# Optimization experiments

Hardware: AMD Instinct MI355X
Metric: run time of the kernel (lower is better)

## Reference

```python
import math
import jax, jax.numpy as jnp
import numpy as np
from jax.scipy.special import xlogy, gammaln

DIM = 768
HEADS = 8
DIM_KEY = 64
DIM_VALUE = 64
NUM_REL_POS_FEATURES = 192
B = 2
N = 2048


def get_positional_embed(seq_len, feature_size):
    # distances: [-n+1, ..., n-1], length 2n-1
    dist = jnp.arange(-seq_len + 1, seq_len).astype(jnp.float32)
    ad = jnp.abs(dist)[:, None]  # [2n-1, 1]
    nb = feature_size // 6  # num basis per class (3 fns, doubled by sign concat)

    # exponential
    max_range = math.log(seq_len) / math.log(2.0)
    half_life = 2.0 ** jnp.linspace(3.0, max_range, nb)  # min_half_life = 3.0
    f_exp = jnp.exp(-math.log(2.0) / half_life[None, :] * ad)

    # central mask
    widths = 2.0 ** jnp.arange(1, nb + 1).astype(jnp.float32) - 1.0
    f_cm = (widths[None, :] > ad).astype(jnp.float32)

    # gamma pdf
    stddev = seq_len / (2.0 * nb)
    start_mean = seq_len / nb
    mean = jnp.linspace(start_mean, float(seq_len), nb)[None, :]
    conc = (mean / stddev) ** 2
    rate = mean / (stddev ** 2)
    log_unnorm = xlogy(conc - 1.0, ad) - rate * ad
    log_norm = gammaln(conc) - conc * jnp.log(rate)
    prob = jnp.exp(log_unnorm - log_norm) + 1e-8
    f_g = prob / jnp.max(prob, axis=-1, keepdims=True)

    emb = jnp.concatenate([f_exp, f_cm, f_g], axis=-1)  # [2n-1, 3*nb]
    emb = jnp.concatenate([emb, jnp.sign(dist)[:, None] * emb], axis=-1)  # [2n-1, 6*nb]
    return emb


def relative_shift(x):
    # x: [b, h, t1, 2*t1 - 1] -> [b, h, t1, t1] via pad/reshape trick
    b, h, t1, t2 = x.shape
    x = jnp.pad(x, ((0, 0), (0, 0), (0, 0), (1, 0)))  # [b,h,t1,t2+1]
    x = x.reshape(b, h, t2 + 1, t1)[:, :, 1:, :].reshape(b, h, t1, t2)
    return x[..., : (t2 + 2) // 2]


def setup_inputs() -> dict:
    key = jax.random.key(0)
    ks = jax.random.split(key, 9)
    dk, dv, h = DIM_KEY, DIM_VALUE, HEADS
    s_in = 1.0 / math.sqrt(DIM)
    s_rel = 1.0 / math.sqrt(NUM_REL_POS_FEATURES)
    s_out = 1.0 / math.sqrt(dv * h)
    return {
        "x": jax.random.normal(ks[0], (B, N, DIM), dtype=jnp.float32),
        # weights stored [in, out] (torch Linear weight transposed)
        "Wq": jax.random.normal(ks[1], (DIM, dk * h), dtype=jnp.float32) * s_in,
        "Wk": jax.random.normal(ks[2], (DIM, dk * h), dtype=jnp.float32) * s_in,
        "Wv": jax.random.normal(ks[3], (DIM, dv * h), dtype=jnp.float32) * s_in,
        "Wrel": jax.random.normal(ks[4], (NUM_REL_POS_FEATURES, dk * h), dtype=jnp.float32) * s_rel,
        # module inits to_out at zeros; use random values for a meaningful baseline
        "Wout": jax.random.normal(ks[5], (dv * h, DIM), dtype=jnp.float32) * s_out,
        "b_out": jax.random.normal(ks[6], (DIM,), dtype=jnp.float32) * 0.01,
        "rel_content_bias": jax.random.normal(ks[7], (1, h, 1, dk), dtype=jnp.float32),
        "rel_pos_bias": jax.random.normal(ks[8], (1, h, 1, dk), dtype=jnp.float32),
    }


def reference(x, Wq, Wk, Wv, Wrel, Wout, b_out, rel_content_bias, rel_pos_bias):
    b, n, _ = x.shape
    h, dk = HEADS, DIM_KEY
    scale = dk ** -0.5

    q = (x @ Wq).reshape(b, n, h, dk).transpose(0, 2, 1, 3) * scale  # [b,h,n,dk]
    k = (x @ Wk).reshape(b, n, h, dk).transpose(0, 2, 1, 3)
    v = (x @ Wv).reshape(b, n, h, -1).transpose(0, 2, 1, 3)  # [b,h,n,dv]

    content_logits = jnp.einsum('bhid,bhjd->bhij', q + rel_content_bias, k)

    positions = get_positional_embed(n, NUM_REL_POS_FEATURES)  # [2n-1, F]
    rel_k = (positions @ Wrel).reshape(2 * n - 1, h, dk).transpose(1, 0, 2)  # [h,2n-1,dk]
    rel_logits = jnp.einsum('bhid,hjd->bhij', q + rel_pos_bias, rel_k)  # [b,h,n,2n-1]
    rel_logits = relative_shift(rel_logits)  # [b,h,n,n]

    attn = jax.nn.softmax(content_logits + rel_logits, axis=-1)
    out = jnp.einsum('bhij,bhjd->bhid', attn, v)  # [b,h,n,dv]
    out = out.transpose(0, 2, 1, 3).reshape(b, n, -1)  # [b,n,h*dv]
    return out @ Wout + b_out
```

## Files before the change

kernel.cpp:

```cpp
#include <hip/hip_runtime.h>
#include <hip/hip_bf16.h>
#include <math.h>
#include <stdint.h>

typedef __hip_bfloat16 bf16;
typedef __attribute__((ext_vector_type(8))) short short8;
typedef __attribute__((ext_vector_type(4))) float f32x4;

#define SEQ   2048
#define NPOS  4095
#define DIMM  768
#define HEADS 8
#define DK    64
#define HD    512
#define BATCH 2
#define BH    16
#define ROWS  4096

#define OB_RELK  ((size_t)0)
#define OB_QC    ((size_t)4194304)
#define OB_QP    ((size_t)8388608)
#define OB_K     ((size_t)12582912)
#define OB_V     ((size_t)16777216)
#define OB_OH    ((size_t)20971520)
#define OB_EMBH  OB_OH
#define OB_EMBL  ((size_t)(OB_OH + 1572864))
#define OB_XH    ((size_t)25165824)
#define OB_XL    ((size_t)31457280)
#define OB_WQKVH ((size_t)37748736)
#define OB_WQKVL ((size_t)40108032)
#define OB_OP    ((size_t)25165824)
#define OB_LP    ((size_t)41943040)
#define OB_WOH   ((size_t)42467328)
#define OB_WOL   ((size_t)43253760)
#define OB_WRH   ((size_t)44040192)
#define OB_WRL   ((size_t)44236800)

__device__ __forceinline__ unsigned f2bf(float f) {
  unsigned u = __float_as_uint(f);
  return (u + 0x7fffu + ((u >> 16) & 1u)) >> 16;
}
__device__ __forceinline__ void split2(float v, unsigned& hb, unsigned& lb) {
  hb = f2bf(v);
  const float back = __uint_as_float(hb << 16);
  lb = f2bf(v - back);
}

__device__ __forceinline__ void cp16(const short* g, short* l) {
  __builtin_amdgcn_global_load_lds(
      (__attribute__((address_space(1))) void*)(uintptr_t)(g),
      (__attribute__((address_space(3))) void*)(uint32_t)(uintptr_t)(l),
      16, 0, 0);
}

__global__ __launch_bounds__(256) void prep_all(
    const float* __restrict__ x,
    const float* __restrict__ Wq, const float* __restrict__ Wk,
    const float* __restrict__ Wv, const float* __restrict__ Wout,
    const float* __restrict__ Wrel,
    short* __restrict__ eh, short* __restrict__ el,
    short* __restrict__ xh, short* __restrict__ xl,
    short* __restrict__ wqkvh, short* __restrict__ wqkvl,
    short* __restrict__ woh, short* __restrict__ wol,
    short* __restrict__ wrh, short* __restrict__ wrl) {
  __shared__ float tile[32][33];
  const int blk = blockIdx.x;
  const int t = threadIdx.x;

  if (blk < 512) {
    const int row = blk * 8 + (t >> 5);
    const int j   = t & 31;
    if (row >= NPOS) {
      for (int c = j; c < 192; c += 32) { eh[(size_t)row * 192 + c] = 0; el[(size_t)row * 192 + c] = 0; }
      return;
    }
    const float dist = (float)(row - (SEQ - 1));
    const float ad   = fabsf(dist);
    const float hl    = exp2f(3.0f + 8.0f * (float)j / 31.0f);
    const float f_exp = exp2f(-ad / hl);
    const float width = exp2f((float)(j + 1)) - 1.0f;
    const float f_cm  = (width > ad) ? 1.0f : 0.0f;
    float prob;
    if (ad > 0.0f) {
      const float c   = 4.0f * (float)((j + 1) * (j + 1));
      const float r   = (float)(j + 1) / 16.0f;
      const float lu  = (c - 1.0f) * logf(ad) - r * ad;
      const float ln_ = lgammaf(c) - c * logf(r);
      prob = expf(lu - ln_) + 1e-8f;
    } else {
      prob = 1e-8f;
    }
    float mx = prob;
    for (int off = 16; off; off >>= 1) mx = fmaxf(mx, __shfl_xor(mx, off, 32));
    const float f_g = prob / mx;
    const float s = (dist > 0.f) ? 1.f : ((dist < 0.f) ? -1.f : 0.f);
    const float vals[6] = {f_exp, f_cm, f_g, s * f_exp, s * f_cm, s * f_g};
    short* ph = eh + (size_t)row * 192;
    short* pl = el + (size_t)row * 192;
#pragma unroll
    for (int q = 0; q < 6; q++) {
      unsigned hb, lb;
      split2(vals[q], hb, lb);
      ph[q * 32 + j] = (short)hb;
      pl[q * 32 + j] = (short)lb;
    }
    return;
  }

  if (blk < 3584) {
    const int i = (blk - 512) * 256 + t;
    const float4 v = ((const float4*)x)[i];
    unsigned h0, l0, h1, l1, h2, l2, h3, l3;
    split2(v.x, h0, l0); split2(v.y, h1, l1); split2(v.z, h2, l2); split2(v.w, h3, l3);
    *(uint2*)&xh[(size_t)i * 4] = make_uint2(h0 | (h1 << 16), h2 | (h3 << 16));
    *(uint2*)&xl[(size_t)i * 4] = make_uint2(l0 | (l1 << 16), l2 | (l3 << 16));
    return;
  }

  const float* src; short* dh; short* dl; int R, C, local;
  if (blk < 3968)      { local = blk - 3584; src = Wq;   dh = wqkvh;               dl = wqkvl;               R = DIMM; C = HD; }
  else if (blk < 4352) { local = blk - 3968; src = Wk;   dh = wqkvh + 512 * DIMM;  dl = wqkvl + 512 * DIMM;  R = DIMM; C = HD; }
  else if (blk < 4736) { local = blk - 4352; src = Wv;   dh = wqkvh + 1024 * DIMM; dl = wqkvl + 1024 * DIMM; R = DIMM; C = HD; }
  else if (blk < 5120) { local = blk - 4736; src = Wout; dh = woh;  dl = wol;  R = HD;  C = DIMM; }
  else                 { local = blk - 5120; src = Wrel; dh = wrh;  dl = wrl;  R = 192; C = HD; }
  const int ctiles = C / 32;
  const int c0 = (local % ctiles) * 32, r0 = (local / ctiles) * 32;
  {
    const int lr = t >> 3, lc = (t & 7) * 4;
    const float4 v = *(const float4*)&src[(size_t)(r0 + lr) * C + c0 + lc];
    tile[lr][lc] = v.x; tile[lr][lc + 1] = v.y; tile[lr][lc + 2] = v.z; tile[lr][lc + 3] = v.w;
  }
  __syncthreads();
  const int nn = t >> 3, kb = (t & 7) * 4;
  unsigned hb[4], lb[4];
#pragma unroll
  for (int e = 0; e < 4; e++) split2(tile[kb + e][nn], hb[e], lb[e]);
  const size_t o = (size_t)(c0 + nn) * R + r0 + kb;
  *(uint2*)&dh[o] = make_uint2(hb[0] | (hb[1] << 16), hb[2] | (hb[3] << 16));
  *(uint2*)&dl[o] = make_uint2(lb[0] | (lb[1] << 16), lb[2] | (lb[3] << 16));
}

__global__ __launch_bounds__(256) void gemm_qr(
    const short* __restrict__ xh, const short* __restrict__ xl,
    const short* __restrict__ wqkvh, const short* __restrict__ wqkvl,
    const short* __restrict__ eh, const short* __restrict__ el,
    const short* __restrict__ wrh, const short* __restrict__ wrl,
    const float* __restrict__ cb, const float* __restrict__ pb,
    bf16* __restrict__ oq, bf16* __restrict__ oqp,
    bf16* __restrict__ ok, short* __restrict__ vtw,
    bf16* __restrict__ relk) {
  __shared__ short AsH[2][128][32];
  __shared__ short AsL[2][128][32];
  __shared__ short BsH[2][128][32];
  __shared__ short BsL[2][128][32];

  const int bx = blockIdx.x;
  const bool isq = bx < 384;
  const int lbx = isq ? bx : bx - 384;
  const int mt = lbx & 31, ntile = lbx >> 5;
  const int m0 = mt * 128, n0 = ntile * 128;
  const int KD = isq ? DIMM : 192;
  const short* Ah = isq ? xh : eh;
  const short* Al = isq ? xl : el;
  const short* Bh = isq ? wqkvh : wrh;
  const short* Bl = isq ? wqkvl : wrl;

  const int t = threadIdx.x, lane = t & 63, w = t >> 6;
  const int quad = lane >> 4, l15 = lane & 15;
  const int wm = (w >> 1) * 64, wn = (w & 1) * 64;

  const int srow = w * 32 + (lane >> 2);
  const int skof = (lane & 3) * 8;

  auto STAGE = [&](int bb, int k0) {
#pragma unroll
    for (int c = 0; c < 2; c++) {
      const size_t ra = (size_t)(m0 + srow + c * 16) * KD + k0 + skof;
      const size_t rb = (size_t)(n0 + srow + c * 16) * KD + k0 + skof;
      cp16(&Ah[ra], &AsH[bb][w * 32 + c * 16][0]);
      cp16(&Al[ra], &AsL[bb][w * 32 + c * 16][0]);
      cp16(&Bh[rb], &BsH[bb][w * 32 + c * 16][0]);
      cp16(&Bl[rb], &BsL[bb][w * 32 + c * 16][0]);
    }
  };

  f32x4 acc[4][4];
#pragma unroll
  for (int i = 0; i < 4; i++)
#pragma unroll
    for (int j = 0; j < 4; j++) acc[i][j] = (f32x4){0.f, 0.f, 0.f, 0.f};

  STAGE(0, 0);
  __syncthreads();

  int bb = 0;
  for (int k0 = 0; k0 < KD; k0 += 32) {
    if (k0 + 32 < KD) STAGE(bb ^ 1, k0 + 32);

    short8 amh[4], aml[4], bnh[4], bnl[4];
#pragma unroll
    for (int i = 0; i < 4; i++) {
      amh[i] = *(const short8*)&AsH[bb][wm + i * 16 + l15][quad * 8];
      aml[i] = *(const short8*)&AsL[bb][wm + i * 16 + l15][quad * 8];
      bnh[i] = *(const short8*)&BsH[bb][wn + i * 16 + l15][quad * 8];
      bnl[i] = *(const short8*)&BsL[bb][wn + i * 16 + l15][quad * 8];
    }
#pragma unroll
    for (int i = 0; i < 4; i++) {
#pragma unroll
      for (int j = 0; j < 4; j++) {
        acc[i][j] = __builtin_amdgcn_mfma_f32_16x16x32_bf16(amh[i], bnh[j], acc[i][j], 0, 0, 0);
        acc[i][j] = __builtin_amdgcn_mfma_f32_16x16x32_bf16(amh[i], bnl[j], acc[i][j], 0, 0, 0);
        acc[i][j] = __builtin_amdgcn_mfma_f32_16x16x32_bf16(aml[i], bnh[j], acc[i][j], 0, 0, 0);
      }
    }

    __syncthreads();
    bb ^= 1;
  }

  if (isq) {
    const int sel = ntile >> 2;
    if (sel == 2) {
#pragma unroll
      for (int i = 0; i < 4; i++) {
#pragma unroll
        for (int j = 0; j < 4; j++) {
          const int n = n0 + wn + j * 16 + l15;
          const int hd_ = n & 511, hh = hd_ >> 6, d = hd_ & 63;
          const int m = m0 + wm + i * 16 + quad * 4;
          const int b = m >> 11, s = m & 2047;
          const int s_swz = s ^ ((d & 7) << 3);
          const uint2 pk = make_uint2(
              f2bf(acc[i][j][0]) | (f2bf(acc[i][j][1]) << 16),
              f2bf(acc[i][j][2]) | (f2bf(acc[i][j][3]) << 16));
          *(uint2*)&vtw[(((size_t)(b * HEADS + hh) * DK + d) * SEQ) + s_swz] = pk;
        }
      }
    } else {
#pragma unroll
      for (int i = 0; i < 4; i++) {
#pragma unroll
        for (int j = 0; j < 4; j++) {
          const int n = n0 + wn + j * 16 + l15;
          const int hd_ = n & 511, hh = hd_ >> 6, d = hd_ & 63;
#pragma unroll
          for (int g = 0; g < 4; g++) {
            const int m = m0 + wm + i * 16 + quad * 4 + g;
            const int b = m >> 11, s = m & 2047;
            const size_t idx = (((size_t)(b * HEADS + hh) * SEQ) + s) * DK + d;
            const float v = acc[i][j][g];
            if (sel == 0) {
              const float sv = v * 0.125f;
              oq[idx]  = __float2bfloat16(sv + cb[hh * DK + d]);
              oqp[idx] = __float2bfloat16(sv + pb[hh * DK + d]);
            } else {
              ok[idx] = __float2bfloat16(v);
            }
          }
        }
      }
    }
  } else {
#pragma unroll
    for (int i = 0; i < 4; i++) {
#pragma unroll
      for (int j = 0; j < 4; j++) {
        const int n = n0 + wn + j * 16 + l15;
        const int hh = n >> 6, d = n & 63;
#pragma unroll
        for (int g = 0; g < 4; g++) {
          const int m = m0 + wm + i * 16 + quad * 4 + g;
          if (m < NPOS)
            relk[((size_t)hh * NPOS + m) * DK + (d ^ ((m & 7) << 3))] =
                __float2bfloat16(acc[i][j][g]);
        }
      }
    }
  }
}

__global__ __launch_bounds__(256) void out_gemm(
    const short* __restrict__ Ahp,
    const short* __restrict__ Bhp, const short* __restrict__ Blp,
    const float* __restrict__ bias, float* __restrict__ ofp) {
  __shared__ short AsH[2][128][32];
  __shared__ short BsH[2][128][32];
  __shared__ short BsL[2][128][32];

  const int t = threadIdx.x, lane = t & 63, w = t >> 6;
  const int quad = lane >> 4, l15 = lane & 15;
  const int wm = (w >> 1) * 64, wn = (w & 1) * 64;
  const int m0 = blockIdx.x * 128, n0 = blockIdx.y * 128;
  const int srow = w * 32 + (lane >> 2);
  const int skof = (lane & 3) * 8;

  auto STAGE = [&](int bb, int k0) {
#pragma unroll
    for (int c = 0; c < 2; c++) {
      const size_t ra = (size_t)(m0 + srow + c * 16) * HD + k0 + skof;
      const size_t rb = (size_t)(n0 + srow + c * 16) * HD + k0 + skof;
      cp16(&Ahp[ra], &AsH[bb][w * 32 + c * 16][0]);
      cp16(&Bhp[rb], &BsH[bb][w * 32 + c * 16][0]);
      cp16(&Blp[rb], &BsL[bb][w * 32 + c * 16][0]);
    }
  };

  f32x4 acc[4][4];
#pragma unroll
  for (int i = 0; i < 4; i++)
#pragma unroll
    for (int j = 0; j < 4; j++) acc[i][j] = (f32x4){0.f, 0.f, 0.f, 0.f};

  STAGE(0, 0);
  __syncthreads();

  int bb = 0;
  for (int k0 = 0; k0 < HD; k0 += 32) {
    if (k0 + 32 < HD) STAGE(bb ^ 1, k0 + 32);

    short8 amh[4], bnh[4], bnl[4];
#pragma unroll
    for (int i = 0; i < 4; i++) {
      amh[i] = *(const short8*)&AsH[bb][wm + i * 16 + l15][quad * 8];
      bnh[i] = *(const short8*)&BsH[bb][wn + i * 16 + l15][quad * 8];
      bnl[i] = *(const short8*)&BsL[bb][wn + i * 16 + l15][quad * 8];
    }
#pragma unroll
    for (int i = 0; i < 4; i++) {
#pragma unroll
      for (int j = 0; j < 4; j++) {
        acc[i][j] = __builtin_amdgcn_mfma_f32_16x16x32_bf16(amh[i], bnh[j], acc[i][j], 0, 0, 0);
        acc[i][j] = __builtin_amdgcn_mfma_f32_16x16x32_bf16(amh[i], bnl[j], acc[i][j], 0, 0, 0);
      }
    }

    __syncthreads();
    bb ^= 1;
  }

#pragma unroll
  for (int i = 0; i < 4; i++) {
#pragma unroll
    for (int j = 0; j < 4; j++) {
      const int n = n0 + wn + j * 16 + l15;
      const float bv = bias[n];
#pragma unroll
      for (int g = 0; g < 4; g++) {
        const int m = m0 + wm + i * 16 + quad * 4 + g;
        ofp[(size_t)m * DIMM + n] = acc[i][j][g] + bv;
      }
    }
  }
}

__global__ __launch_bounds__(256) void attn_mfma4(
    const short* __restrict__ qc, const short* __restrict__ qp,
    const short* __restrict__ kg, const short* __restrict__ vt,
    const short* __restrict__ relk,
    float* __restrict__ Op, float* __restrict__ Lp) {
  __shared__ __align__(16) short RelR[128 * 64];
  __shared__ __align__(16) short VtB[2][64 * 64];
  __shared__ __align__(16) short Pw[4][16][64];

  const int bid = blockIdx.x;
  const int swz = (bid & 7) * 128 + (bid >> 3);
  const int i0  = (swz & 31) * 64;
  const int bh  = (swz >> 5) & 15;
  const int z   = swz >> 9;
  const int h   = bh & 7;
  const int jb  = z * (SEQ / 2);

  const int t    = threadIdx.x;
  const int lane = t & 63;
  const int w    = t >> 6;
  const int quad = lane >> 4;
  const int l15  = lane & 15;
  const int x    = (l15 & 7) << 3;

  short8 qcA[2], qpA[2];
  {
    const size_t qrow = ((size_t)bh * SEQ + i0 + w * 16 + l15) * DK + quad * 8;
    qcA[0] = *(const short8*)(qc + qrow);
    qcA[1] = *(const short8*)(qc + qrow + 32);
    qpA[0] = *(const short8*)(qp + qrow);
    qpA[1] = *(const short8*)(qp + qrow + 32);
  }

  int idxg[4]; bool selg[4];
#pragma unroll
  for (int g = 0; g < 4; g++) {
    const int r = quad * 4 + g;
    idxg[g] = (((lane & 48) | ((l15 + 15 - r) & 15)) << 2);
    selg[g] = (l15 <= r);
  }

  short8 ones8;
#pragma unroll
  for (int e = 0; e < 8; e++) ones8[e] = (short)0x3F80;

  f32x4 oacc[4];
#pragma unroll
  for (int dt = 0; dt < 4; dt++) oacc[dt] = (f32x4){0.f, 0.f, 0.f, 0.f};
  f32x4 lacc = (f32x4){0.f, 0.f, 0.f, 0.f};

  const short* kbase = kg + (size_t)bh * SEQ * DK;
  const short* vbase = vt + (size_t)bh * DK * SEQ;
  const short* rbase = relk + ((size_t)(h * NPOS + 1984 - i0)) * DK;

  const int rb_w = 48 - 16 * w;

  auto STAGEV = [&](int nxt, int j0n) {
#pragma unroll
    for (int cc = 0; cc < 2; cc++) {
      const int c = w * 2 + cc;
      cp16(vbase + (size_t)(c * 8 + (lane >> 3)) * SEQ + j0n + (lane & 7) * 8,
           &VtB[nxt][c * 512]);
    }
  };

#pragma unroll
  for (int cc = 0; cc < 4; cc++) {
    const int c = w + cc * 4;
    if (c < 14)
      cp16(rbase + (size_t)(jb + 16) * DK + c * 512 + lane * 8, &RelR[1024 + c * 512]);
  }
  STAGEV(0, jb);
  f32x4 bpp_carry;
  {
    const short* rl = rbase + (size_t)(jb + rb_w + l15) * DK;
    short8 b0 = *(const short8*)(rl + ((quad * 8) ^ x));
    short8 b1 = *(const short8*)(rl + ((quad * 8 + 32) ^ x));
    f32x4 a = (f32x4){0.f, 0.f, 0.f, 0.f};
    a = __builtin_amdgcn_mfma_f32_16x16x32_bf16(qpA[0], b0, a, 0, 0, 0);
    a = __builtin_amdgcn_mfma_f32_16x16x32_bf16(qpA[1], b1, a, 0, 0, 0);
#pragma unroll
    for (int g = 0; g < 4; g++)
      bpp_carry[g] = __int_as_float(__builtin_amdgcn_ds_bpermute(idxg[g], __float_as_int(a[g])));
  }
  __syncthreads();

  int cur = 0;
  for (int jt = 0; jt < 16; jt++) {
    const int j0 = jb + jt * 64;
    const int rowoff = (jt & 1) * 64;

    if (jt < 15) STAGEV(cur ^ 1, j0 + 64);

    f32x4 sacc[4];
#pragma unroll
    for (int nt = 0; nt < 4; nt++) {
      const short* kr = kbase + (size_t)(j0 + nt * 16 + l15) * DK + quad * 8;
      short8 b0 = *(const short8*)kr;
      short8 b1 = *(const short8*)(kr + 32);
      f32x4 a = (f32x4){0.f, 0.f, 0.f, 0.f};
      a = __builtin_amdgcn_mfma_f32_16x16x32_bf16(qcA[0], b0, a, 0, 0, 0);
      a = __builtin_amdgcn_mfma_f32_16x16x32_bf16(qcA[1], b1, a, 0, 0, 0);
      sacc[nt] = a;
    }

    f32x4 bpp = bpp_carry;

#pragma unroll
    for (int nt = 0; nt < 4; nt++) {
      f32x4 rcur;
      {
        const int slot = (rowoff + 16 + rb_w + nt * 16 + l15) & 127;
        const short* rl = &RelR[slot * 64];
        short8 b0 = *(const short8*)(rl + ((quad * 8) ^ x));
        short8 b1 = *(const short8*)(rl + ((quad * 8 + 32) ^ x));
        f32x4 a = (f32x4){0.f, 0.f, 0.f, 0.f};
        a = __builtin_amdgcn_mfma_f32_16x16x32_bf16(qpA[0], b0, a, 0, 0, 0);
        a = __builtin_amdgcn_mfma_f32_16x16x32_bf16(qpA[1], b1, a, 0, 0, 0);
        rcur = a;
      }
      f32x4 bpc;
#pragma unroll
      for (int g = 0; g < 4; g++)
        bpc[g] = __int_as_float(__builtin_amdgcn_ds_bpermute(idxg[g], __float_as_int(rcur[g])));
#pragma unroll
      for (int g = 0; g < 4; g++) {
        const float relv = selg[g] ? bpp[g] : bpc[g];
        const float s = sacc[nt][g] + relv;
        const float p = __expf(s - 12.0f);
        const int prow = quad * 4 + g;
        Pw[w][prow][(nt * 16 + l15) ^ ((prow & 7) << 3)] = (short)f2bf(p);
      }
      bpp = bpc;
    }
    bpp_carry = bpp;

    __syncthreads();

    if (jt < 15) {
      const short* rsrc = rbase + (size_t)(j0 + 128) * DK;
#pragma unroll
      for (int cc = 0; cc < 2; cc++) {
        const int c = w * 2 + cc;
        cp16(rsrc + c * 512 + lane * 8, &RelR[rowoff * 64 + c * 512]);
      }
    }

#pragma unroll
    for (int ks = 0; ks < 2; ks++) {
      short8 pA = *(const short8*)&Pw[w][l15][(ks * 32 + quad * 8) ^ x];
      lacc = __builtin_amdgcn_mfma_f32_16x16x32_bf16(pA, ones8, lacc, 0, 0, 0);
#pragma unroll
      for (int dt = 0; dt < 4; dt++) {
        const short* vl = &VtB[cur][(dt * 16 + l15) * 64 + ((ks * 32 + quad * 8) ^ x)];
        short8 vB = *(const short8*)vl;
        oacc[dt] = __builtin_amdgcn_mfma_f32_16x16x32_bf16(pA, vB, oacc[dt], 0, 0, 0);
      }
    }

    cur ^= 1;
    __syncthreads();
  }

  const size_t obase = ((size_t)(z * BH + bh) * SEQ + i0 + w * 16);
#pragma unroll
  for (int g = 0; g < 4; g++) {
    const int r = quad * 4 + g;
#pragma unroll
    for (int dt = 0; dt < 4; dt++)
      Op[(obase + r) * DK + dt * 16 + l15] = oacc[dt][g];
    if (l15 == 0) Lp[obase + r] = lacc[g];
  }
}

__global__ void merge_kernel(const float* __restrict__ Op, const float* __restrict__ Lp,
                             bf16* __restrict__ oh) {
  const int gid = blockIdx.x * 256 + threadIdx.x;
  const int m = gid >> 7;
  const int n0 = (gid & 127) * 4;
  const int b = m >> 11, s = m & 2047;
  const int hh = n0 >> 6, d0 = n0 & 63;
  const int bh = b * HEADS + hh;
  const float l = Lp[(size_t)bh * SEQ + s] + Lp[((size_t)BH + bh) * SEQ + s];
  const float inv = 1.0f / l;
  const float4 o0 = *(const float4*)&Op[((size_t)bh * SEQ + s) * DK + d0];
  const float4 o1 = *(const float4*)&Op[(((size_t)BH + bh) * SEQ + s) * DK + d0];
  *(uint2*)&oh[(size_t)m * HD + n0] = make_uint2(
      f2bf((o0.x + o1.x) * inv) | (f2bf((o0.y + o1.y) * inv) << 16),
      f2bf((o0.z + o1.z) * inv) | (f2bf((o0.w + o1.w) * inv) << 16));
}

extern "C" void kernel_launch(void* const* d_in, const int* in_sizes, int n_in,
                              void* d_out, int out_size, void* d_ws, size_t ws_size,
                              hipStream_t stream) {
  (void)in_sizes; (void)n_in; (void)out_size; (void)ws_size;
  const float* x    = (const float*)d_in[0];
  const float* Wq   = (const float*)d_in[1];
  const float* Wk   = (const float*)d_in[2];
  const float* Wv   = (const float*)d_in[3];
  const float* Wrel = (const float*)d_in[4];
  const float* Wout = (const float*)d_in[5];
  const float* bout = (const float*)d_in[6];
  const float* cb   = (const float*)d_in[7];
  const float* pb   = (const float*)d_in[8];
  float* out = (float*)d_out;

  char* ws = (char*)d_ws;
  bf16*  relk = (bf16*)(ws + OB_RELK);
  bf16*  qc   = (bf16*)(ws + OB_QC);
  bf16*  qp   = (bf16*)(ws + OB_QP);
  bf16*  kk   = (bf16*)(ws + OB_K);
  short* vt   = (short*)(ws + OB_V);
  bf16*  oh   = (bf16*)(ws + OB_OH);
  float* Opb  = (float*)(ws + OB_OP);
  float* Lpb  = (float*)(ws + OB_LP);
  short* embh = (short*)(ws + OB_EMBH);
  short* embl = (short*)(ws + OB_EMBL);
  short* xh   = (short*)(ws + OB_XH);
  short* xl   = (short*)(ws + OB_XL);
  short* wqh  = (short*)(ws + OB_WQKVH);
  short* wql  = (short*)(ws + OB_WQKVL);
  short* woh  = (short*)(ws + OB_WOH);
  short* wol  = (short*)(ws + OB_WOL);
  short* wrh  = (short*)(ws + OB_WRH);
  short* wrl  = (short*)(ws + OB_WRL);

  hipLaunchKernelGGL(prep_all, dim3(5216), dim3(256), 0, stream,
                     x, Wq, Wk, Wv, Wout, Wrel,
                     embh, embl, xh, xl, wqh, wql, woh, wol, wrh, wrl);
  hipLaunchKernelGGL(gemm_qr, dim3(512), dim3(256), 0, stream,
                     xh, xl, wqh, wql, embh, embl, wrh, wrl,
                     cb, pb, qc, qp, kk, vt, relk);
  hipLaunchKernelGGL(attn_mfma4, dim3(1024), dim3(256), 0, stream,
                     (const short*)qc, (const short*)qp, (const short*)kk,
                     (const short*)vt, (const short*)relk, Opb, Lpb);
  hipLaunchKernelGGL(merge_kernel, dim3(ROWS * (HD / 4) / 256), dim3(256), 0, stream,
                     Opb, Lpb, oh);
  hipLaunchKernelGGL(out_gemm, dim3(32, 6), dim3(256), 0, stream,
                     (const short*)oh, woh, wol, bout, out);
}
```

Baseline: 215.1 us.

## Fuse split-KV merge into attention block and swizzle QKV GEMM blocks

Each attention block now has 512 threads in two groups of four waves, each group covering half of the key range for the same query tile. The two partial outputs are combined through shared memory, and the normalized bf16 result is written directly, so the separate merge kernel and its fp32 partial buffers go away. The V tile is now single-buffered per half and its next load is issued after the barrier, which may reduce load/compute overlap. The Q/K/V/rel GEMM also gets a block-index swizzle to change how tiles are spread across the grid.

```diff
diff --git a/kernel.cpp b/kernel.cpp
--- a/kernel.cpp
+++ b/kernel.cpp
@@ -29,8 +29,6 @@
 #define OB_XL    ((size_t)31457280)
 #define OB_WQKVH ((size_t)37748736)
 #define OB_WQKVL ((size_t)40108032)
-#define OB_OP    ((size_t)25165824)
-#define OB_LP    ((size_t)41943040)
 #define OB_WOH   ((size_t)42467328)
 #define OB_WOL   ((size_t)43253760)
 #define OB_WRH   ((size_t)44040192)
@@ -154,7 +152,8 @@
   __shared__ short BsH[2][128][32];
   __shared__ short BsL[2][128][32];
 
-  const int bx = blockIdx.x;
+  const int bxr = blockIdx.x;
+  const int bx = (bxr & 7) * 64 + (bxr >> 3);
   const bool isq = bx < 384;
   const int lbx = isq ? bx : bx - 384;
   const int mt = lbx & 31, ntile = lbx >> 5;
@@ -354,33 +353,34 @@
   }
 }
 
-__global__ __launch_bounds__(256) void attn_mfma4(
+__global__ __launch_bounds__(512) void attn_mfma4(
     const short* __restrict__ qc, const short* __restrict__ qp,
     const short* __restrict__ kg, const short* __restrict__ vt,
     const short* __restrict__ relk,
-    float* __restrict__ Op, float* __restrict__ Lp) {
-  __shared__ __align__(16) short RelR[128 * 64];
-  __shared__ __align__(16) short VtB[2][64 * 64];
-  __shared__ __align__(16) short Pw[4][16][64];
+    short* __restrict__ oh) {
+  __shared__ __align__(16) short RelR[2][128 * 64];
+  __shared__ __align__(16) short VtS[2][64 * 64];
+  __shared__ __align__(16) short Pw[8][16][64];
 
   const int bid = blockIdx.x;
-  const int swz = (bid & 7) * 128 + (bid >> 3);
+  const int swz = (bid & 7) * 64 + (bid >> 3);
   const int i0  = (swz & 31) * 64;
-  const int bh  = (swz >> 5) & 15;
-  const int z   = swz >> 9;
+  const int bh  = swz >> 5;
   const int h   = bh & 7;
-  const int jb  = z * (SEQ / 2);
 
   const int t    = threadIdx.x;
   const int lane = t & 63;
   const int w    = t >> 6;
+  const int wl   = w & 3;
+  const int half = w >> 2;
+  const int jb   = half * (SEQ / 2);
   const int quad = lane >> 4;
   const int l15  = lane & 15;
   const int x    = (l15 & 7) << 3;
 
   short8 qcA[2], qpA[2];
   {
-    const size_t qrow = ((size_t)bh * SEQ + i0 + w * 16 + l15) * DK + quad * 8;
+    const size_t qrow = ((size_t)bh * SEQ + i0 + wl * 16 + l15) * DK + quad * 8;
     qcA[0] = *(const short8*)(qc + qrow);
     qcA[1] = *(const short8*)(qc + qrow + 32);
     qpA[0] = *(const short8*)(qp + qrow);
@@ -408,24 +408,25 @@
   const short* vbase = vt + (size_t)bh * DK * SEQ;
   const short* rbase = relk + ((size_t)(h * NPOS + 1984 - i0)) * DK;
 
-  const int rb_w = 48 - 16 * w;
-
-  auto STAGEV = [&](int nxt, int j0n) {
+  const int rb_w = 48 - 16 * wl;
+
+  auto STAGEV = [&](int j0n) {
 #pragma unroll
     for (int cc = 0; cc < 2; cc++) {
-      const int c = w * 2 + cc;
+      const int c = wl * 2 + cc;
       cp16(vbase + (size_t)(c * 8 + (lane >> 3)) * SEQ + j0n + (lane & 7) * 8,
-           &VtB[nxt][c * 512]);
+           &VtS[half][c * 512]);
     }
   };
 
 #pragma unroll
   for (int cc = 0; cc < 4; cc++) {
-    const int c = w + cc * 4;
+    const int c = wl + cc * 4;
     if (c < 14)
-      cp16(rbase + (size_t)(jb + 16) * DK + c * 512 + lane * 8, &RelR[1024 + c * 512]);
-  }
-  STAGEV(0, jb);
+      cp16(rbase + (size_t)(jb + 16) * DK + c * 512 + lane * 8,
+           &RelR[half][1024 + c * 512]);
+  }
+  STAGEV(jb);
   f32x4 bpp_carry;
   {
     const short* rl = rbase + (size_t)(jb + rb_w + l15) * DK;
@@ -440,12 +441,9 @@
   }
   __syncthreads();
 
-  int cur = 0;
   for (int jt = 0; jt < 16; jt++) {
     const int j0 = jb + jt * 64;
     const int rowoff = (jt & 1) * 64;
-
-    if (jt < 15) STAGEV(cur ^ 1, j0 + 64);
 
     f32x4 sacc[4];
 #pragma unroll
@@ -466,7 +464,7 @@
       f32x4 rcur;
       {
         const int slot = (rowoff + 16 + rb_w + nt * 16 + l15) & 127;
-        const short* rl = &RelR[slot * 64];
+        const short* rl = &RelR[half][slot * 64];
         short8 b0 = *(const short8*)(rl + ((quad * 8) ^ x));
         short8 b1 = *(const short8*)(rl + ((quad * 8 + 32) ^ x));
         f32x4 a = (f32x4){0.f, 0.f, 0.f, 0.f};
@@ -496,8 +494,8 @@
       const short* rsrc = rbase + (size_t)(j0 + 128) * DK;
 #pragma unroll
       for (int cc = 0; cc < 2; cc++) {
-        const int c = w * 2 + cc;
-        cp16(rsrc + c * 512 + lane * 8, &RelR[rowoff * 64 + c * 512]);
+        const int c = wl * 2 + cc;
+        cp16(rsrc + c * 512 + lane * 8, &RelR[half][rowoff * 64 + c * 512]);
       }
     }
 
@@ -507,42 +505,43 @@
       lacc = __builtin_amdgcn_mfma_f32_16x16x32_bf16(pA, ones8, lacc, 0, 0, 0);
 #pragma unroll
       for (int dt = 0; dt < 4; dt++) {
-        const short* vl = &VtB[cur][(dt * 16 + l15) * 64 + ((ks * 32 + quad * 8) ^ x)];
+        const short* vl = &VtS[half][(dt * 16 + l15) * 64 + ((ks * 32 + quad * 8) ^ x)];
         short8 vB = *(const short8*)vl;
         oacc[dt] = __builtin_amdgcn_mfma_f32_16x16x32_bf16(pA, vB, oacc[dt], 0, 0, 0);
       }
     }
 
-    cur ^= 1;
     __syncthreads();
-  }
-
-  const size_t obase = ((size_t)(z * BH + bh) * SEQ + i0 + w * 16);
-#pragma unroll
-  for (int g = 0; g < 4; g++) {
-    const int r = quad * 4 + g;
-#pragma unroll
-    for (int dt = 0; dt < 4; dt++)
-      Op[(obase + r) * DK + dt * 16 + l15] = oacc[dt][g];
-    if (l15 == 0) Lp[obase + r] = lacc[g];
-  }
-}
-
-__global__ void merge_kernel(const float* __restrict__ Op, const float* __restrict__ Lp,
-                             bf16* __restrict__ oh) {
-  const int gid = blockIdx.x * 256 + threadIdx.x;
-  const int m = gid >> 7;
-  const int n0 = (gid & 127) * 4;
-  const int b = m >> 11, s = m & 2047;
-  const int hh = n0 >> 6, d0 = n0 & 63;
-  const int bh = b * HEADS + hh;
-  const float l = Lp[(size_t)bh * SEQ + s] + Lp[((size_t)BH + bh) * SEQ + s];
-  const float inv = 1.0f / l;
-  const float4 o0 = *(const float4*)&Op[((size_t)bh * SEQ + s) * DK + d0];
-  const float4 o1 = *(const float4*)&Op[(((size_t)BH + bh) * SEQ + s) * DK + d0];
-  *(uint2*)&oh[(size_t)m * HD + n0] = make_uint2(
-      f2bf((o0.x + o1.x) * inv) | (f2bf((o0.y + o1.y) * inv) << 16),
-      f2bf((o0.z + o1.z) * inv) | (f2bf((o0.w + o1.w) * inv) << 16));
+    if (jt < 15) STAGEV(j0 + 64);
+  }
+
+  float* oscr = (float*)&VtS[0][0];
+  float* lscr = (float*)&RelR[0][0];
+  if (w >= 4) {
+#pragma unroll
+    for (int g = 0; g < 4; g++) {
+      const int r = quad * 4 + g;
+#pragma unroll
+      for (int dt = 0; dt < 4; dt++)
+        oscr[(wl * 16 + r) * 64 + dt * 16 + l15] = oacc[dt][g];
+      if (l15 == 0) lscr[wl * 16 + r] = lacc[g];
+    }
+  }
+  __syncthreads();
+  if (w < 4) {
+    const int b = bh >> 3, hh = bh & 7;
+#pragma unroll
+    for (int g = 0; g < 4; g++) {
+      const int r = quad * 4 + g;
+      const float linv = 1.0f / (lacc[g] + lscr[wl * 16 + r]);
+      const size_t mrow = (size_t)(b * SEQ + i0 + wl * 16 + r) * HD + hh * 64;
+#pragma unroll
+      for (int dt = 0; dt < 4; dt++) {
+        const float o = oacc[dt][g] + oscr[(wl * 16 + r) * 64 + dt * 16 + l15];
+        oh[mrow + dt * 16 + l15] = (short)f2bf(o * linv);
+      }
+    }
+  }
 }
 
 extern "C" void kernel_launch(void* const* d_in, const int* in_sizes, int n_in,
@@ -566,9 +565,7 @@
   bf16*  qp   = (bf16*)(ws + OB_QP);
   bf16*  kk   = (bf16*)(ws + OB_K);
   short* vt   = (short*)(ws + OB_V);
-  bf16*  oh   = (bf16*)(ws + OB_OH);
-  float* Opb  = (float*)(ws + OB_OP);
-  float* Lpb  = (float*)(ws + OB_LP);
+  short* oh   = (short*)(ws + OB_OH);
   short* embh = (short*)(ws + OB_EMBH);
   short* embl = (short*)(ws + OB_EMBL);
   short* xh   = (short*)(ws + OB_XH);
@@ -586,11 +583,9 @@
   hipLaunchKernelGGL(gemm_qr, dim3(512), dim3(256), 0, stream,
                      xh, xl, wqh, wql, embh, embl, wrh, wrl,
                      cb, pb, qc, qp, kk, vt, relk);
-  hipLaunchKernelGGL(attn_mfma4, dim3(1024), dim3(256), 0, stream,
+  hipLaunchKernelGGL(attn_mfma4, dim3(512), dim3(512), 0, stream,
                      (const short*)qc, (const short*)qp, (const short*)kk,
-                     (const short*)vt, (const short*)relk, Opb, Lpb);
-  hipLaunchKernelGGL(merge_kernel, dim3(ROWS * (HD / 4) / 256), dim3(256), 0, stream,
-                     Opb, Lpb, oh);
+                     (const short*)vt, (const short*)relk, oh);
   hipLaunchKernelGGL(out_gemm, dim3(32, 6), dim3(256), 0, stream,
                      (const short*)oh, woh, wol, bout, out);
 }
```

New measurement: 214.9 us. No clear change (-0.1%).
